# Kernel tuning notes

Hardware: AMD Instinct MI355X
Metric: run time of the kernel (lower is better)

The kernel has to match this reference:

```python
import jax, jax.numpy as jnp
import numpy as np

N, E, D, NHID, NOUT, G = 100000, 600000, 128, 512, 768, 2048
EPS = 1e-5

def _lin_init(k, fi, fo):
    s = 1.0 / np.sqrt(fi)
    kw, kb = jax.random.split(k)
    W = jax.random.uniform(kw, (fi, fo), jnp.float32, -s, s)
    b = jax.random.uniform(kb, (fo,), jnp.float32, -s, s)
    return W, b

def setup_inputs():
    key = jax.random.key(0)
    ks = jax.random.split(key, 16)
    inp = {}
    inp['x'] = jax.random.normal(ks[0], (N, D), jnp.float32)
    inp['edge_index'] = jax.random.randint(ks[1], (2, E), 0, N, jnp.int32)
    inp['batch'] = jnp.sort(jax.random.randint(ks[2], (N,), 0, G, jnp.int32))
    # 3 GCN layers + GAT attention layer + 4 MLP linears
    inp['W1'], inp['b1'] = _lin_init(ks[3], D, D)
    inp['W2'], inp['b2'] = _lin_init(ks[4], D, D)
    inp['W3'], inp['b3'] = _lin_init(ks[5], D, D)
    inp['Wa'], inp['ba'] = _lin_init(ks[6], D, D)
    ka1, ka2 = jax.random.split(ks[7])
    inp['a_src'] = jax.random.normal(ka1, (D,), jnp.float32) * 0.1
    inp['a_dst'] = jax.random.normal(ka2, (D,), jnp.float32) * 0.1
    # batchnorm affine params (4 BNs)
    for i, nm in enumerate(['g1', 'g2', 'g3', 'ga']):
        inp[nm] = jnp.ones((D,), jnp.float32)
        inp['be' + nm[1:]] = jnp.zeros((D,), jnp.float32)
    inp['Wl1'], inp['bl1'] = _lin_init(ks[8], D, NHID)
    inp['Wl2'], inp['bl2'] = _lin_init(ks[9], NHID, NHID)
    inp['Wl3'], inp['bl3'] = _lin_init(ks[10], NHID, NHID)
    inp['Wl4'], inp['bl4'] = _lin_init(ks[11], NHID, NOUT)
    inp['gln'] = jnp.ones((NOUT,), jnp.float32)
    inp['bln'] = jnp.zeros((NOUT,), jnp.float32)
    return inp

def _bn(x, g, b):
    # training-mode batchnorm over node dim (biased variance, like torch)
    mu = jnp.mean(x, axis=0)
    var = jnp.var(x, axis=0)
    return (x - mu) * jax.lax.rsqrt(var + EPS) * g + b

def _forward(x, edge_index, batch, W1, b1, g1, be1, W2, b2, g2, be2, W3, b3, g3, be3,
             Wa, ba, a_src, a_dst, ga, bea, Wl1, bl1, Wl2, bl2, Wl3, bl3, Wl4, bl4, gln, bln):
    loop = jnp.arange(N, dtype=edge_index.dtype)
    src = jnp.concatenate([edge_index[0], loop])  # [E+N] with self-loops
    dst = jnp.concatenate([edge_index[1], loop])
    deg = jax.ops.segment_sum(jnp.ones_like(dst, jnp.float32), dst, num_segments=N)
    dinv = jax.lax.rsqrt(deg)  # deg >= 1 thanks to self-loops
    norm = (dinv[src] * dinv[dst])[:, None]  # [E+N, 1]

    def gcn(h, W, b):
        h = h @ W
        return jax.ops.segment_sum(h[src] * norm, dst, num_segments=N) + b

    x = jax.nn.relu(_bn(gcn(x, W1, b1), g1, be1)) + x
    x = jax.nn.relu(_bn(gcn(x, W2, b2), g2, be2)) + x
    x = jax.nn.relu(_bn(gcn(x, W3, b3), g3, be3)) + x

    # GATConv, heads=1: edge logit = LeakyReLU(a_src.h_j + a_dst.h_i), softmax over dst
    h = x @ Wa
    al = h @ a_src  # [N]
    ar = h @ a_dst
    e = jax.nn.leaky_relu(al[src] + ar[dst], 0.2)  # [E+N]
    m = jax.ops.segment_max(e, dst, num_segments=N)
    ee = jnp.exp(e - m[dst])
    denom = jax.ops.segment_sum(ee, dst, num_segments=N)
    alpha = (ee / denom[dst])[:, None]
    x = jax.ops.segment_sum(alpha * h[src], dst, num_segments=N) + ba
    x = jax.nn.relu(_bn(x, ga, bea))

    # global_add_pool
    x = jax.ops.segment_sum(x, batch, num_segments=G)  # [G, D]

    x = jax.nn.relu(x @ Wl1 + bl1)
    x = jax.nn.relu(x @ Wl2 + bl2)
    x = jax.nn.relu(x @ Wl3 + bl3)
    x = x @ Wl4 + bl4
    mu = jnp.mean(x, axis=-1, keepdims=True)
    var = jnp.var(x, axis=-1, keepdims=True)
    return (x - mu) * jax.lax.rsqrt(var + EPS) * gln + bln

def reference(x, edge_index, batch, W1, b1, g1, be1, W2, b2, g2, be2, W3, b3, g3, be3,
              Wa, ba, a_src, a_dst, ga, bea, Wl1, bl1, Wl2, bl2, Wl3, bl3, Wl4, bl4, gln, bln):
    return _forward(x, edge_index, batch, W1, b1, g1, be1, W2, b2, g2, be2, W3, b3, g3, be3,
                    Wa, ba, a_src, a_dst, ga, bea, Wl1, bl1, Wl2, bl2, Wl3, bl3, Wl4, bl4, gln, bln)
```

## Files before the change

kernel.cpp:

```cpp
#include <hip/hip_runtime.h>
#include <cstdint>
#include <cstddef>

#define CDIV(a,b) (((a)+(b)-1)/(b))

constexpr int N_ = 100000;
constexpr int E_ = 600000;
constexpr int D_ = 128;
constexpr int G_ = 2048;
constexpr int NHID_ = 512;
constexpr int NOUT_ = 768;
constexpr float EPS_ = 1e-5f;
constexpr int AGG_BLOCKS = 2048;

typedef short bf16x8 __attribute__((ext_vector_type(8)));
typedef float f32x4 __attribute__((ext_vector_type(4)));

__device__ __forceinline__ float wave_sum(float v){
#pragma unroll
  for (int m = 32; m; m >>= 1) v += __shfl_xor(v, m, 64);
  return v;
}
__device__ __forceinline__ float lrelu02(float v){ return v > 0.f ? v : 0.2f * v; }
__device__ __forceinline__ unsigned short f2bf(float f){
  unsigned u = __float_as_uint(f);
  u += 0x7FFF + ((u >> 16) & 1);
  return (unsigned short)(u >> 16);
}
__device__ __forceinline__ float bflo(unsigned u){ return __uint_as_float(u << 16); }
__device__ __forceinline__ float bfhi(unsigned u){ return __uint_as_float(u & 0xFFFF0000u); }

__device__ __forceinline__ float4 unplo(uint4 u){ return make_float4(bflo(u.x), bflo(u.y), bflo(u.z), bflo(u.w)); }
__device__ __forceinline__ float4 unphi(uint4 u){ return make_float4(bfhi(u.x), bfhi(u.y), bfhi(u.z), bfhi(u.w)); }
__device__ __forceinline__ float4 bnrelu4(float4 v, float4 sc, float4 sh){
  return make_float4(fmaxf(v.x*sc.x+sh.x, 0.f), fmaxf(v.y*sc.y+sh.y, 0.f),
                     fmaxf(v.z*sc.z+sh.z, 0.f), fmaxf(v.w*sc.w+sh.w, 0.f));
}
__device__ __forceinline__ float4 add4(float4 a, float4 b){
  return make_float4(a.x+b.x, a.y+b.y, a.z+b.z, a.w+b.w);
}
__device__ __forceinline__ uint4 pk4(float4 lo, float4 hi){
  uint4 u;
  u.x = (unsigned)f2bf(lo.x) | ((unsigned)f2bf(hi.x) << 16);
  u.y = (unsigned)f2bf(lo.y) | ((unsigned)f2bf(hi.y) << 16);
  u.z = (unsigned)f2bf(lo.z) | ((unsigned)f2bf(hi.z) << 16);
  u.w = (unsigned)f2bf(lo.w) | ((unsigned)f2bf(hi.w) << 16);
  return u;
}
__device__ __forceinline__ bf16x8 mkaf(float4 lo, float4 hi){
  bf16x8 a;
  a[0]=(short)f2bf(lo.x); a[1]=(short)f2bf(lo.y); a[2]=(short)f2bf(lo.z); a[3]=(short)f2bf(lo.w);
  a[4]=(short)f2bf(hi.x); a[5]=(short)f2bf(hi.y); a[6]=(short)f2bf(hi.z); a[7]=(short)f2bf(hi.w);
  return a;
}
__device__ __forceinline__ bf16x8 mkaf_u(uint4 u){
  bf16x8 a;
  a[0]=(short)(u.x & 0xFFFF); a[4]=(short)(u.x >> 16);
  a[1]=(short)(u.y & 0xFFFF); a[5]=(short)(u.y >> 16);
  a[2]=(short)(u.z & 0xFFFF); a[6]=(short)(u.z >> 16);
  a[3]=(short)(u.w & 0xFFFF); a[7]=(short)(u.w >> 16);
  return a;
}

__global__ void k_count(const int* __restrict__ dst, int* __restrict__ cnt){
  int e = blockIdx.x * 256 + threadIdx.x;
  if (e < E_) atomicAdd(&cnt[dst[e]], 1);
}

__global__ void k_scan1(const int* __restrict__ cnt, int* __restrict__ ro, int* __restrict__ bs,
                        float* __restrict__ dinv){
  __shared__ int s[256];
  int tid = threadIdx.x;
  int i = blockIdx.x * 256 + tid;
  int v = (i < N_) ? cnt[i] : 0;
  s[tid] = v; __syncthreads();
  for (int off = 1; off < 256; off <<= 1){
    int add = (tid >= off) ? s[tid - off] : 0;
    __syncthreads();
    s[tid] += add;
    __syncthreads();
  }
  if (i < N_){
    ro[i] = s[tid] - v;
    dinv[i] = rsqrtf((float)(v + 1));
  }
  if (tid == 255) bs[blockIdx.x] = s[255];
}

__global__ void k_scan2(int* __restrict__ bs, int nb){
  __shared__ int s[512];
  int t = threadIdx.x;
  int v = (t < nb) ? bs[t] : 0;
  s[t] = v; __syncthreads();
  for (int off = 1; off < 512; off <<= 1){
    int a = (t >= off) ? s[t - off] : 0;
    __syncthreads();
    s[t] += a;
    __syncthreads();
  }
  if (t < nb) bs[t] = s[t] - v;
}

__global__ void k_scan3(int* __restrict__ ro, const int* __restrict__ bs){
  int i = blockIdx.x * 256 + threadIdx.x;
  if (i < N_) ro[i] += bs[i >> 8];
  if (i == N_) ro[N_] = E_;
}

__global__ void k_fill(const int* __restrict__ src, const int* __restrict__ dst,
                       const int* __restrict__ ro, int* __restrict__ cur, int* __restrict__ csr){
  int e = blockIdx.x * 256 + threadIdx.x;
  if (e < E_){
    int d = dst[e];
    int p = atomicAdd(&cur[d], 1);
    csr[ro[d] + p] = src[e];
  }
}

__global__ void k_bounds(const int* __restrict__ batch, int* __restrict__ gs){
  int g = blockIdx.x * 256 + threadIdx.x;
  if (g > G_) return;
  int lo = 0, hi = N_;
  while (lo < hi){ int mid = (lo + hi) >> 1; if (batch[mid] < g) lo = mid + 1; else hi = mid; }
  gs[g] = lo;
}

struct WprepArgs {
  const float* W[8];
  short* Wt[8];
  int K[8];
  int N[8];
  int ofs[9];
};

__global__ void k_wprep_all(WprepArgs a){
  int i = blockIdx.x * 256 + threadIdx.x;
  if (i >= a.ofs[8]) return;
  int m = 0;
  while (i >= a.ofs[m + 1]) ++m;
  int li = i - a.ofs[m];
  int K = a.K[m], Nn = a.N[m];
  int KT = K >> 5;
  int g = li & 3, t = (li >> 2) % KT, c = li / (KT * 4);
  short* o = a.Wt[m] + (size_t)li * 8;
  const float* W = a.W[m];
#pragma unroll
  for (int j = 0; j < 8; ++j){
    int k = t * 32 + (j >> 2) * 16 + g * 4 + (j & 3);
    o[j] = (short)f2bf(W[(size_t)k * Nn + c]);
  }
}

template<bool XB, bool RB>
__global__ __launch_bounds__(256) void k_mm_mfma(const void* __restrict__ Xin,
                                                 const short* __restrict__ Wt,
                                                 unsigned* __restrict__ hout,
                                                 const float* __restrict__ ss,
                                                 const void* __restrict__ resin,
                                                 unsigned* __restrict__ xnew,
                                                 const float* __restrict__ prescale,
                                                 const float* __restrict__ asrc,
                                                 const float* __restrict__ adst,
                                                 float* __restrict__ al_out,
                                                 float* __restrict__ ar_out){
  int lane = threadIdx.x & 63, wid = threadIdx.x >> 6;
  int cl = lane & 15, g = lane >> 4;
  int rw0 = blockIdx.x * 64 + wid * 16;
  int arow = rw0 + cl;
  bool rv = arow < N_;
  int rm = rv ? arow : 0;
  bool has_res = resin != nullptr;

  uint4 xu[4]; float4 xf[8];
  uint4 ru[4]; float4 rf[8];
  if (XB){
    const uint4* Xr = (const uint4*)((const unsigned*)Xin + (size_t)rm * 64);
#pragma unroll
    for (int t = 0; t < 4; ++t) xu[t] = Xr[t*4 + g];
  } else {
    const float4* Xr = (const float4*)((const float*)Xin + (size_t)rm * 128);
#pragma unroll
    for (int t = 0; t < 4; ++t){ xf[2*t] = Xr[t*8 + g]; xf[2*t+1] = Xr[t*8 + g + 4]; }
  }
  if (has_res){
    if (RB){
      const uint4* Rr = (const uint4*)((const unsigned*)resin + (size_t)rm * 64);
#pragma unroll
      for (int t = 0; t < 4; ++t) ru[t] = Rr[t*4 + g];
    } else {
      const float4* Rr = (const float4*)((const float*)resin + (size_t)rm * 128);
#pragma unroll
      for (int t = 0; t < 4; ++t){ rf[2*t] = Rr[t*8 + g]; rf[2*t+1] = Rr[t*8 + g + 4]; }
    }
  }
  __builtin_amdgcn_sched_barrier(0);

  bf16x8 af[4];
#pragma unroll
  for (int t = 0; t < 4; ++t){
    float4 lo, hi;
    if (XB){ lo = unplo(xu[t]); hi = unphi(xu[t]); }
    else    { lo = xf[2*t];     hi = xf[2*t+1];    }
    if (ss){
      int f0 = t * 32 + g * 4;
      float4 sc0 = *(const float4*)&ss[f0],      sh0 = *(const float4*)&ss[128 + f0];
      float4 sc1 = *(const float4*)&ss[f0 + 16], sh1 = *(const float4*)&ss[128 + f0 + 16];
      lo = bnrelu4(lo, sc0, sh0); hi = bnrelu4(hi, sc1, sh1);
      if (has_res){
        if (RB){ lo = add4(lo, unplo(ru[t])); hi = add4(hi, unphi(ru[t])); }
        else    { lo = add4(lo, rf[2*t]);     hi = add4(hi, rf[2*t+1]);    }
      }
      if (xnew && rv) *(uint4*)(xnew + (size_t)arow * 64 + t*16 + g*4) = pk4(lo, hi);
    }
    af[t] = mkaf(lo, hi);
  }

  f32x4 acc[8];
#pragma unroll
  for (int j = 0; j < 8; ++j) acc[j] = (f32x4){0,0,0,0};
#pragma unroll
  for (int t = 0; t < 4; ++t){
#pragma unroll
    for (int j = 0; j < 8; ++j){
      int c = j * 16 + cl;
      bf16x8 bf = *(const bf16x8*)(Wt + ((size_t)c * 16 + t * 4 + g) * 8);
      acc[j] = __builtin_amdgcn_mfma_f32_16x16x32_bf16(af[t], bf, acc[j], 0, 0, 0);
    }
  }

#pragma unroll
  for (int r = 0; r < 4; ++r){
    int row = rw0 + g * 4 + r;
    if (row < N_){
      float psc = prescale ? prescale[row] : 1.f;
#pragma unroll
      for (int jp = 0; jp < 4; ++jp){
        unsigned lo = f2bf(acc[2*jp][r] * psc);
        unsigned hi = f2bf(acc[2*jp+1][r] * psc);
        hout[(size_t)row * 64 + jp * 16 + cl] = (hi << 16) | lo;
      }
    }
  }

  if (al_out){
    float pal[4] = {0,0,0,0}, par[4] = {0,0,0,0};
#pragma unroll
    for (int j = 0; j < 8; ++j){
      float as_ = asrc[j * 16 + cl], ad_ = adst[j * 16 + cl];
#pragma unroll
      for (int r = 0; r < 4; ++r){ pal[r] += acc[j][r] * as_; par[r] += acc[j][r] * ad_; }
    }
#pragma unroll
    for (int m = 1; m < 16; m <<= 1)
#pragma unroll
      for (int r = 0; r < 4; ++r){
        pal[r] += __shfl_xor(pal[r], m, 64);
        par[r] += __shfl_xor(par[r], m, 64);
      }
    if (cl == 0){
#pragma unroll
      for (int r = 0; r < 4; ++r){
        int row = rw0 + g * 4 + r;
        if (row < N_){ al_out[row] = pal[r]; ar_out[row] = par[r]; }
      }
    }
  }
}

__global__ __launch_bounds__(256) void k_gcn_agg2(const unsigned* __restrict__ hbf, const int* __restrict__ ro,
                          const int* __restrict__ csr, const float* __restrict__ dinv,
                          const float* __restrict__ bias, unsigned* __restrict__ outb,
                          float4* __restrict__ pbuf){
  int wid = threadIdx.x >> 6, lane = threadIdx.x & 63;
  int f0 = 32 * (lane >> 4) + (lane & 15), f1 = f0 + 16;
  float bb0 = bias[f0], bb1 = bias[f1];
  float S0 = 0.f, S1 = 0.f, Q0 = 0.f, Q1 = 0.f;
  for (int node = blockIdx.x * 4 + wid; node < N_; node += AGG_BLOCKS * 4){
    int s0 = ro[node], s1 = ro[node + 1];
    int deg = s1 - s0;
    float di = dinv[node];
    unsigned us = hbf[(size_t)node * 64 + lane];
    float a0 = bflo(us), a1 = bfhi(us);
    if (deg <= 64){
      int sidx = (lane < deg) ? csr[s0 + lane] : 0;
      int j = 0;
      for (; j + 4 <= deg; j += 4){
        int sa = __shfl(sidx, j, 64),   sb = __shfl(sidx, j+1, 64);
        int sc = __shfl(sidx, j+2, 64), sd = __shfl(sidx, j+3, 64);
        unsigned ua = hbf[(size_t)sa*64+lane], ub = hbf[(size_t)sb*64+lane];
        unsigned uc = hbf[(size_t)sc*64+lane], ud = hbf[(size_t)sd*64+lane];
        a0 += bflo(ua) + bflo(ub) + bflo(uc) + bflo(ud);
        a1 += bfhi(ua) + bfhi(ub) + bfhi(uc) + bfhi(ud);
      }
      for (; j < deg; ++j){
        int s = __shfl(sidx, j, 64);
        unsigned u = hbf[(size_t)s*64+lane];
        a0 += bflo(u); a1 += bfhi(u);
      }
    } else {
      for (int base = s0; base < s1; base += 64){
        int c = min(64, s1 - base);
        int sidx = (lane < c) ? csr[base + lane] : 0;
        for (int j = 0; j < c; ++j){
          int s = __shfl(sidx, j, 64);
          unsigned u = hbf[(size_t)s*64+lane];
          a0 += bflo(u); a1 += bfhi(u);
        }
      }
    }
    float o0 = di * a0 + bb0;
    float o1 = di * a1 + bb1;
    outb[(size_t)node * 64 + lane] = (unsigned)f2bf(o0) | ((unsigned)f2bf(o1) << 16);
    S0 += o0; S1 += o1; Q0 += o0*o0; Q1 += o1*o1;
  }
  __shared__ float4 sred[4][64];
  sred[wid][lane] = make_float4(S0, S1, Q0, Q1);
  __syncthreads();
  if (wid == 0){
    float4 t = sred[0][lane];
    float4 u1 = sred[1][lane], u2 = sred[2][lane], u3 = sred[3][lane];
    t.x += u1.x + u2.x + u3.x;
    t.y += u1.y + u2.y + u3.y;
    t.z += u1.z + u2.z + u3.z;
    t.w += u1.w + u2.w + u3.w;
    pbuf[(size_t)blockIdx.x * 64 + lane] = t;
  }
}

__global__ __launch_bounds__(256) void k_gat_agg2(const unsigned* __restrict__ hbf, const int* __restrict__ ro,
                          const int* __restrict__ csr, const float* __restrict__ al,
                          const float* __restrict__ ar, const float* __restrict__ bias,
                          unsigned* __restrict__ outb, float4* __restrict__ pbuf){
  int wid = threadIdx.x >> 6, lane = threadIdx.x & 63;
  int f0 = 32 * (lane >> 4) + (lane & 15), f1 = f0 + 16;
  float bb0 = bias[f0], bb1 = bias[f1];
  float S0 = 0.f, S1 = 0.f, Q0 = 0.f, Q1 = 0.f;
  for (int node = blockIdx.x * 4 + wid; node < N_; node += AGG_BLOCKS * 4){
    int s0 = ro[node], s1 = ro[node + 1];
    int deg = s1 - s0;
    float ari = ar[node], ali = al[node];
    float pself = __expf(lrelu02(ali + ari));
    unsigned uself = hbf[(size_t)node * 64 + lane];
    float h0 = bflo(uself), h1 = bfhi(uself);
    float a0, a1;
    if (deg <= 64){
      int sidx = 0; float p = 0.f;
      if (lane < deg){ sidx = csr[s0 + lane]; p = __expf(lrelu02(al[sidx] + ari)); }
      float invd = 1.f / (wave_sum(p) + pself);
      float wl = p * invd;
      float wsf = pself * invd;
      a0 = wsf * h0; a1 = wsf * h1;
      int j = 0;
      for (; j + 4 <= deg; j += 4){
        int sa = __shfl(sidx, j, 64),   sb = __shfl(sidx, j+1, 64);
        int sc = __shfl(sidx, j+2, 64), sd = __shfl(sidx, j+3, 64);
        float wa = __shfl(wl, j, 64),   wb = __shfl(wl, j+1, 64);
        float wc = __shfl(wl, j+2, 64), wd = __shfl(wl, j+3, 64);
        unsigned ua = hbf[(size_t)sa*64+lane], ub = hbf[(size_t)sb*64+lane];
        unsigned uc = hbf[(size_t)sc*64+lane], ud = hbf[(size_t)sd*64+lane];
        a0 += wa*bflo(ua) + wb*bflo(ub) + wc*bflo(uc) + wd*bflo(ud);
        a1 += wa*bfhi(ua) + wb*bfhi(ub) + wc*bfhi(uc) + wd*bfhi(ud);
      }
      for (; j < deg; ++j){
        int s = __shfl(sidx, j, 64); float w = __shfl(wl, j, 64);
        unsigned u = hbf[(size_t)s*64+lane];
        a0 += w*bflo(u); a1 += w*bfhi(u);
      }
    } else {
      float denom = pself;
      for (int base = s0; base < s1; base += 64){
        int c = min(64, s1 - base);
        float p = 0.f;
        if (lane < c) p = __expf(lrelu02(al[csr[base + lane]] + ari));
        denom += wave_sum(p);
      }
      float invd = 1.f / denom;
      float wsf = pself * invd;
      a0 = wsf * h0; a1 = wsf * h1;
      for (int base = s0; base < s1; base += 64){
        int c = min(64, s1 - base);
        int sidx = 0; float wl = 0.f;
        if (lane < c){ sidx = csr[base + lane]; wl = __expf(lrelu02(al[sidx] + ari)) * invd; }
        for (int j = 0; j < c; ++j){
          int s = __shfl(sidx, j, 64); float w = __shfl(wl, j, 64);
          unsigned u = hbf[(size_t)s*64+lane];
          a0 += w*bflo(u); a1 += w*bfhi(u);
        }
      }
    }
    float o0 = a0 + bb0, o1 = a1 + bb1;
    outb[(size_t)node * 64 + lane] = (unsigned)f2bf(o0) | ((unsigned)f2bf(o1) << 16);
    S0 += o0; S1 += o1; Q0 += o0*o0; Q1 += o1*o1;
  }
  __shared__ float4 sred[4][64];
  sred[wid][lane] = make_float4(S0, S1, Q0, Q1);
  __syncthreads();
  if (wid == 0){
    float4 t = sred[0][lane];
    float4 u1 = sred[1][lane], u2 = sred[2][lane], u3 = sred[3][lane];
    t.x += u1.x + u2.x + u3.x;
    t.y += u1.y + u2.y + u3.y;
    t.z += u1.z + u2.z + u3.z;
    t.w += u1.w + u2.w + u3.w;
    pbuf[(size_t)blockIdx.x * 64 + lane] = t;
  }
}

__global__ void k_bn_reduce(const float4* __restrict__ pbuf, const float* __restrict__ g,
                            const float* __restrict__ be, float* __restrict__ ss){
  int c = blockIdx.x;
  int f0 = 32 * (c >> 4) + (c & 15), f1 = f0 + 16;
  float4 a = make_float4(0.f, 0.f, 0.f, 0.f);
  for (int r = threadIdx.x; r < AGG_BLOCKS; r += 256){
    float4 v = pbuf[(size_t)r * 64 + c];
    a.x += v.x; a.y += v.y; a.z += v.z; a.w += v.w;
  }
  __shared__ float4 s[256];
  s[threadIdx.x] = a; __syncthreads();
  for (int off = 128; off; off >>= 1){
    if (threadIdx.x < off){
      float4 o = s[threadIdx.x + off];
      s[threadIdx.x].x += o.x; s[threadIdx.x].y += o.y;
      s[threadIdx.x].z += o.z; s[threadIdx.x].w += o.w;
    }
    __syncthreads();
  }
  if (threadIdx.x == 0){
    float4 t = s[0];
    float inv_n = 1.f / (float)N_;
    float mean0 = t.x * inv_n, mean1 = t.y * inv_n;
    float var0 = fmaxf(t.z * inv_n - mean0 * mean0, 0.f);
    float var1 = fmaxf(t.w * inv_n - mean1 * mean1, 0.f);
    float sc0 = g[f0] * rsqrtf(var0 + EPS_);
    float sc1 = g[f1] * rsqrtf(var1 + EPS_);
    ss[f0] = sc0; ss[f1] = sc1;
    ss[128 + f0] = be[f0] - mean0 * sc0;
    ss[128 + f1] = be[f1] - mean1 * sc1;
  }
}

__global__ void k_pool2(const unsigned* __restrict__ xn, const int* __restrict__ gs,
                        const float* __restrict__ ss, unsigned* __restrict__ pooled){
  int g = blockIdx.x, f = threadIdx.x & 127, half = threadIdx.x >> 7;
  int idx = ((f >> 5) << 4) | (f & 15);
  int hi = (f >> 4) & 1;
  int s = gs[g], e = gs[g + 1];
  float sc = ss[f], sh = ss[128 + f];
  float a = 0.f;
  for (int n = s + half; n < e; n += 2){
    unsigned u = xn[(size_t)n * 64 + idx];
    float v = hi ? bfhi(u) : bflo(u);
    a += fmaxf(v * sc + sh, 0.f);
  }
  __shared__ float red[256];
  red[threadIdx.x] = a; __syncthreads();
  if (half == 0 && hi == 0){
    float vlo = red[f] + red[f + 128];
    float vhi = red[f + 16] + red[f + 16 + 128];
    pooled[(size_t)g * 64 + idx] = (unsigned)f2bf(vlo) | ((unsigned)f2bf(vhi) << 16);
  }
}

template<int K, bool RELU, bool OUTF32>
__global__ __launch_bounds__(256) void k_gemm_mfma(const unsigned* __restrict__ A,
                                                   const short* __restrict__ Wt,
                                                   const float* __restrict__ bias,
                                                   void* __restrict__ Cout, int Ncols){
  constexpr int KT = K >> 5;
  int lane = threadIdx.x & 63, wid = threadIdx.x >> 6;
  int cl = lane & 15, g = lane >> 4;
  int row0 = blockIdx.y * 64 + wid * 16;
  int cb = blockIdx.x;
  int arow = row0 + cl;
  const uint4* Ar = (const uint4*)(A + (size_t)arow * (K / 2));

  f32x4 acc[8];
#pragma unroll
  for (int j = 0; j < 8; ++j) acc[j] = (f32x4){0,0,0,0};

  for (int t = 0; t < KT; ++t){
    bf16x8 af = mkaf_u(Ar[t*4 + g]);
#pragma unroll
    for (int j = 0; j < 8; ++j){
      int c = cb * 128 + j * 16 + cl;
      bf16x8 bf = *(const bf16x8*)(Wt + (((size_t)c * KT + t) * 4 + g) * 8);
      acc[j] = __builtin_amdgcn_mfma_f32_16x16x32_bf16(af, bf, acc[j], 0, 0, 0);
    }
  }

  if (OUTF32){
    float* C = (float*)Cout;
#pragma unroll
    for (int r = 0; r < 4; ++r){
      int row = row0 + g * 4 + r;
#pragma unroll
      for (int j = 0; j < 8; ++j){
        int c = cb * 128 + j * 16 + cl;
        float v = acc[j][r] + bias[c];
        if (RELU) v = fmaxf(v, 0.f);
        C[(size_t)row * Ncols + c] = v;
      }
    }
  } else {
    unsigned* C = (unsigned*)Cout;
#pragma unroll
    for (int r = 0; r < 4; ++r){
      int row = row0 + g * 4 + r;
#pragma unroll
      for (int jp = 0; jp < 4; ++jp){
        int clo = cb * 128 + jp * 32 + cl;
        float vlo = acc[2*jp][r] + bias[clo];
        float vhi = acc[2*jp+1][r] + bias[clo + 16];
        if (RELU){ vlo = fmaxf(vlo, 0.f); vhi = fmaxf(vhi, 0.f); }
        C[(size_t)row * (Ncols / 2) + (cb * 4 + jp) * 16 + cl] =
            (unsigned)f2bf(vlo) | ((unsigned)f2bf(vhi) << 16);
      }
    }
  }
}

__global__ void k_layernorm(const float* __restrict__ xin, const float* __restrict__ g,
                            const float* __restrict__ b, float* __restrict__ out){
  __shared__ float red[8];
  int row = blockIdx.x, tid = threadIdx.x;
  float v0 = xin[(size_t)row*768 + tid];
  float v1 = xin[(size_t)row*768 + tid + 256];
  float v2 = xin[(size_t)row*768 + tid + 512];
  float s = v0 + v1 + v2;
  float q = v0*v0 + v1*v1 + v2*v2;
  s = wave_sum(s); q = wave_sum(q);
  int wid = tid >> 6;
  if ((tid & 63) == 0){ red[wid] = s; red[4 + wid] = q; }
  __syncthreads();
  if (tid == 0){
    float ts = red[0] + red[1] + red[2] + red[3];
    float tq = red[4] + red[5] + red[6] + red[7];
    float mean = ts / 768.f;
    float var = tq / 768.f - mean * mean;
    red[0] = mean; red[1] = rsqrtf(fmaxf(var, 0.f) + EPS_);
  }
  __syncthreads();
  float mean = red[0], inv = red[1];
  out[(size_t)row*768 + tid]       = (v0 - mean) * inv * g[tid]       + b[tid];
  out[(size_t)row*768 + tid + 256] = (v1 - mean) * inv * g[tid + 256] + b[tid + 256];
  out[(size_t)row*768 + tid + 512] = (v2 - mean) * inv * g[tid + 512] + b[tid + 512];
}

extern "C" void kernel_launch(void* const* d_in, const int* in_sizes, int n_in,
                              void* d_out, int out_size, void* d_ws, size_t ws_size,
                              hipStream_t stream){
  const float* x     = (const float*)d_in[0];
  const int*   ei    = (const int*)d_in[1];
  const int*   src   = ei;
  const int*   dst   = ei + E_;
  const int*   batch = (const int*)d_in[2];
  const float* W1 = (const float*)d_in[3];  const float* b1 = (const float*)d_in[4];
  const float* W2 = (const float*)d_in[5];  const float* b2 = (const float*)d_in[6];
  const float* W3 = (const float*)d_in[7];  const float* b3 = (const float*)d_in[8];
  const float* Wa = (const float*)d_in[9];  const float* ba = (const float*)d_in[10];
  const float* a_src = (const float*)d_in[11]; const float* a_dst = (const float*)d_in[12];
  const float* g1 = (const float*)d_in[13]; const float* be1 = (const float*)d_in[14];
  const float* g2 = (const float*)d_in[15]; const float* be2 = (const float*)d_in[16];
  const float* g3 = (const float*)d_in[17]; const float* be3 = (const float*)d_in[18];
  const float* ga = (const float*)d_in[19]; const float* bea = (const float*)d_in[20];
  const float* Wl1 = (const float*)d_in[21]; const float* bl1 = (const float*)d_in[22];
  const float* Wl2 = (const float*)d_in[23]; const float* bl2 = (const float*)d_in[24];
  const float* Wl3 = (const float*)d_in[25]; const float* bl3 = (const float*)d_in[26];
  const float* Wl4 = (const float*)d_in[27]; const float* bl4 = (const float*)d_in[28];
  const float* gln = (const float*)d_in[29]; const float* bln = (const float*)d_in[30];
  float* out = (float*)d_out;

  char* base = (char*)d_ws;
  size_t off = 0;
  auto alloc = [&](size_t bytes)->char*{
    char* p = base + off;
    off += (bytes + 255) & ~(size_t)255;
    return p;
  };
  int*   cnt    = (int*)  alloc((size_t)N_ * 4);
  float* dinv   = (float*)alloc((size_t)N_ * 4);
  int*   ro     = (int*)  alloc((size_t)(N_ + 1) * 4);
  int*   bs     = (int*)  alloc(512 * 4);
  int*   cur    = (int*)  alloc((size_t)N_ * 4);
  int*   csr    = (int*)  alloc((size_t)E_ * 4);
  int*   gstart = (int*)  alloc((size_t)(G_ + 1) * 4);
  float* al     = (float*)alloc((size_t)N_ * 4);
  float* ar     = (float*)alloc((size_t)N_ * 4);
  float* ss     = (float*)alloc(256 * 4);
  float4* pbuf  = (float4*)alloc((size_t)AGG_BLOCKS * 64 * 16);
  short* wt1    = (short*)alloc((size_t)128 * 128 * 2);
  short* wt2    = (short*)alloc((size_t)128 * 128 * 2);
  short* wt3    = (short*)alloc((size_t)128 * 128 * 2);
  short* wta    = (short*)alloc((size_t)128 * 128 * 2);
  short* wtl1   = (short*)alloc((size_t)128 * NHID_ * 2);
  short* wtl2   = (short*)alloc((size_t)NHID_ * NHID_ * 2);
  short* wtl3   = (short*)alloc((size_t)NHID_ * NHID_ * 2);
  short* wtl4   = (short*)alloc((size_t)NHID_ * NOUT_ * 2);
  unsigned* bufH  = (unsigned*)alloc((size_t)N_ * 64 * 4);
  unsigned* bufYb = (unsigned*)alloc((size_t)N_ * 64 * 4);
  unsigned* xresb = (unsigned*)alloc((size_t)N_ * 64 * 4);
  unsigned* pooled= (unsigned*)alloc((size_t)G_ * 64 * 4);
  unsigned* m1b   = (unsigned*)alloc((size_t)G_ * (NHID_/2) * 4);
  unsigned* m2b   = (unsigned*)alloc((size_t)G_ * (NHID_/2) * 4);
  float* m4     = (float*)alloc((size_t)G_ * NOUT_ * 4);
  (void)ws_size; (void)in_sizes; (void)n_in; (void)out_size;

  const int nbE = CDIV(E_, 256), nbN = CDIV(N_, 256);
  const int MMB = CDIV(N_, 64);

  hipMemsetAsync(cnt, 0, (size_t)N_ * 4, stream);
  k_count<<<nbE, 256, 0, stream>>>(dst, cnt);
  k_scan1<<<nbN, 256, 0, stream>>>(cnt, ro, bs, dinv);
  k_scan2<<<1, 512, 0, stream>>>(bs, nbN);
  k_scan3<<<CDIV(N_ + 1, 256), 256, 0, stream>>>(ro, bs);
  hipMemsetAsync(cur, 0, (size_t)N_ * 4, stream);
  k_fill<<<nbE, 256, 0, stream>>>(src, dst, ro, cur, csr);
  k_bounds<<<CDIV(G_ + 1, 256), 256, 0, stream>>>(batch, gstart);

  {
    WprepArgs a;
    const float* Ws[8] = {W1, W2, W3, Wa, Wl1, Wl2, Wl3, Wl4};
    short* Wts[8] = {wt1, wt2, wt3, wta, wtl1, wtl2, wtl3, wtl4};
    int Ks[8] = {128,128,128,128, 128, NHID_, NHID_, NHID_};
    int Ns[8] = {128,128,128,128, NHID_, NHID_, NHID_, NOUT_};
    int run = 0;
    for (int m = 0; m < 8; ++m){
      a.W[m] = Ws[m]; a.Wt[m] = Wts[m]; a.K[m] = Ks[m]; a.N[m] = Ns[m];
      a.ofs[m] = run;
      run += Ns[m] * (Ks[m] >> 5) * 4;
    }
    a.ofs[8] = run;
    k_wprep_all<<<CDIV(run, 256), 256, 0, stream>>>(a);
  }

  k_mm_mfma<false,false><<<MMB, 256, 0, stream>>>(x, wt1, bufH, nullptr, nullptr, nullptr,
                                                  dinv, nullptr, nullptr, nullptr, nullptr);
  k_gcn_agg2<<<AGG_BLOCKS, 256, 0, stream>>>(bufH, ro, csr, dinv, b1, bufYb, pbuf);
  k_bn_reduce<<<64, 256, 0, stream>>>(pbuf, g1, be1, ss);
  k_mm_mfma<true,false><<<MMB, 256, 0, stream>>>(bufYb, wt2, bufH, ss, x, xresb,
                                                 dinv, nullptr, nullptr, nullptr, nullptr);
  k_gcn_agg2<<<AGG_BLOCKS, 256, 0, stream>>>(bufH, ro, csr, dinv, b2, bufYb, pbuf);
  k_bn_reduce<<<64, 256, 0, stream>>>(pbuf, g2, be2, ss);
  k_mm_mfma<true,true><<<MMB, 256, 0, stream>>>(bufYb, wt3, bufH, ss, xresb, xresb,
                                                dinv, nullptr, nullptr, nullptr, nullptr);
  k_gcn_agg2<<<AGG_BLOCKS, 256, 0, stream>>>(bufH, ro, csr, dinv, b3, bufYb, pbuf);
  k_bn_reduce<<<64, 256, 0, stream>>>(pbuf, g3, be3, ss);
  k_mm_mfma<true,true><<<MMB, 256, 0, stream>>>(bufYb, wta, bufH, ss, xresb, nullptr,
                                                nullptr, a_src, a_dst, al, ar);
  k_gat_agg2<<<AGG_BLOCKS, 256, 0, stream>>>(bufH, ro, csr, al, ar, ba, bufYb, pbuf);
  k_bn_reduce<<<64, 256, 0, stream>>>(pbuf, ga, bea, ss);
  k_pool2<<<G_, 256, 0, stream>>>(bufYb, gstart, ss, pooled);
  k_gemm_mfma<128, true, false><<<dim3(NHID_/128, G_/64), 256, 0, stream>>>(pooled, wtl1, bl1, m1b, NHID_);
  k_gemm_mfma<512, true, false><<<dim3(NHID_/128, G_/64), 256, 0, stream>>>(m1b, wtl2, bl2, m2b, NHID_);
  k_gemm_mfma<512, true, false><<<dim3(NHID_/128, G_/64), 256, 0, stream>>>(m2b, wtl3, bl3, m1b, NHID_);
  k_gemm_mfma<512, false, true><<<dim3(NOUT_/128, G_/64), 256, 0, stream>>>(m1b, wtl4, bl4, m4, NOUT_);
  k_layernorm<<<G_, 256, 0, stream>>>(m4, gln, bln, out);
}
```

Measured before the change: 547.6 us.

## Make node GEMM persistent with register double-buffered prefetch of next tile

The per-node 128x128 MFMA GEMM kernel now launches a fixed grid of 521 blocks. Each block loops over 64-row tiles and prefetches the next tile's input and residual rows into registers while it computes the current one. This is meant to hide global load latency behind MFMA and epilogue work, and to cut block launch overhead. In exchange it doubles the register footprint for input buffers, which may lower occupancy, and with 1563 tiles over 521 blocks each block does exactly three iterations.

New measurement: 557.2 us. Within noise of the previous version (+1.7%).

```diff
diff --git a/kernel.cpp b/kernel.cpp
--- a/kernel.cpp
+++ b/kernel.cpp
@@ -12,6 +12,8 @@
 constexpr int NOUT_ = 768;
 constexpr float EPS_ = 1e-5f;
 constexpr int AGG_BLOCKS = 2048;
+constexpr int MM_NT = CDIV(N_, 64);
+constexpr int MM_GRID = 521;
 
 typedef short bf16x8 __attribute__((ext_vector_type(8)));
 typedef float f32x4 __attribute__((ext_vector_type(4)));
@@ -150,6 +152,38 @@
     o[j] = (short)f2bf(W[(size_t)k * Nn + c]);
   }
 }
+
+#define MM_LOADX(bt, xu, xf)                                                        \
+  do {                                                                              \
+    int arow_ = (bt) * 64 + wid * 16 + cl;                                          \
+    int rm_ = arow_ < N_ ? arow_ : 0;                                               \
+    if (XB){                                                                        \
+      const uint4* Xr_ = (const uint4*)((const unsigned*)Xin + (size_t)rm_ * 64);   \
+      _Pragma("unroll")                                                             \
+      for (int t_ = 0; t_ < 4; ++t_) xu[t_] = Xr_[t_*4 + g];                        \
+    } else {                                                                        \
+      const float4* Xr_ = (const float4*)((const float*)Xin + (size_t)rm_ * 128);   \
+      _Pragma("unroll")                                                             \
+      for (int t_ = 0; t_ < 4; ++t_){ xf[2*t_] = Xr_[t_*8 + g]; xf[2*t_+1] = Xr_[t_*8 + g + 4]; } \
+    }                                                                               \
+  } while(0)
+
+#define MM_LOADR(bt, ru, rf)                                                        \
+  do {                                                                              \
+    if (has_res){                                                                   \
+      int arow_ = (bt) * 64 + wid * 16 + cl;                                        \
+      int rm_ = arow_ < N_ ? arow_ : 0;                                             \
+      if (RB){                                                                      \
+        const uint4* Rr_ = (const uint4*)((const unsigned*)resin + (size_t)rm_ * 64);\
+        _Pragma("unroll")                                                           \
+        for (int t_ = 0; t_ < 4; ++t_) ru[t_] = Rr_[t_*4 + g];                      \
+      } else {                                                                      \
+        const float4* Rr_ = (const float4*)((const float*)resin + (size_t)rm_ * 128);\
+        _Pragma("unroll")                                                           \
+        for (int t_ = 0; t_ < 4; ++t_){ rf[2*t_] = Rr_[t_*8 + g]; rf[2*t_+1] = Rr_[t_*8 + g + 4]; } \
+      }                                                                             \
+    }                                                                               \
+  } while(0)
 
 template<bool XB, bool RB>
 __global__ __launch_bounds__(256) void k_mm_mfma(const void* __restrict__ Xin,
@@ -165,105 +199,105 @@
                                                  float* __restrict__ ar_out){
   int lane = threadIdx.x & 63, wid = threadIdx.x >> 6;
   int cl = lane & 15, g = lane >> 4;
-  int rw0 = blockIdx.x * 64 + wid * 16;
-  int arow = rw0 + cl;
-  bool rv = arow < N_;
-  int rm = rv ? arow : 0;
   bool has_res = resin != nullptr;
 
-  uint4 xu[4]; float4 xf[8];
-  uint4 ru[4]; float4 rf[8];
-  if (XB){
-    const uint4* Xr = (const uint4*)((const unsigned*)Xin + (size_t)rm * 64);
-#pragma unroll
-    for (int t = 0; t < 4; ++t) xu[t] = Xr[t*4 + g];
-  } else {
-    const float4* Xr = (const float4*)((const float*)Xin + (size_t)rm * 128);
-#pragma unroll
-    for (int t = 0; t < 4; ++t){ xf[2*t] = Xr[t*8 + g]; xf[2*t+1] = Xr[t*8 + g + 4]; }
-  }
-  if (has_res){
-    if (RB){
-      const uint4* Rr = (const uint4*)((const unsigned*)resin + (size_t)rm * 64);
-#pragma unroll
-      for (int t = 0; t < 4; ++t) ru[t] = Rr[t*4 + g];
-    } else {
-      const float4* Rr = (const float4*)((const float*)resin + (size_t)rm * 128);
-#pragma unroll
-      for (int t = 0; t < 4; ++t){ rf[2*t] = Rr[t*8 + g]; rf[2*t+1] = Rr[t*8 + g + 4]; }
-    }
-  }
-  __builtin_amdgcn_sched_barrier(0);
-
-  bf16x8 af[4];
-#pragma unroll
-  for (int t = 0; t < 4; ++t){
-    float4 lo, hi;
-    if (XB){ lo = unplo(xu[t]); hi = unphi(xu[t]); }
-    else    { lo = xf[2*t];     hi = xf[2*t+1];    }
-    if (ss){
-      int f0 = t * 32 + g * 4;
-      float4 sc0 = *(const float4*)&ss[f0],      sh0 = *(const float4*)&ss[128 + f0];
-      float4 sc1 = *(const float4*)&ss[f0 + 16], sh1 = *(const float4*)&ss[128 + f0 + 16];
-      lo = bnrelu4(lo, sc0, sh0); hi = bnrelu4(hi, sc1, sh1);
-      if (has_res){
-        if (RB){ lo = add4(lo, unplo(ru[t])); hi = add4(hi, unphi(ru[t])); }
-        else    { lo = add4(lo, rf[2*t]);     hi = add4(hi, rf[2*t+1]);    }
-      }
-      if (xnew && rv) *(uint4*)(xnew + (size_t)arow * 64 + t*16 + g*4) = pk4(lo, hi);
-    }
-    af[t] = mkaf(lo, hi);
-  }
-
-  f32x4 acc[8];
-#pragma unroll
-  for (int j = 0; j < 8; ++j) acc[j] = (f32x4){0,0,0,0};
-#pragma unroll
-  for (int t = 0; t < 4; ++t){
-#pragma unroll
-    for (int j = 0; j < 8; ++j){
-      int c = j * 16 + cl;
-      bf16x8 bf = *(const bf16x8*)(Wt + ((size_t)c * 16 + t * 4 + g) * 8);
-      acc[j] = __builtin_amdgcn_mfma_f32_16x16x32_bf16(af[t], bf, acc[j], 0, 0, 0);
-    }
-  }
-
-#pragma unroll
-  for (int r = 0; r < 4; ++r){
-    int row = rw0 + g * 4 + r;
-    if (row < N_){
-      float psc = prescale ? prescale[row] : 1.f;
-#pragma unroll
-      for (int jp = 0; jp < 4; ++jp){
-        unsigned lo = f2bf(acc[2*jp][r] * psc);
-        unsigned hi = f2bf(acc[2*jp+1][r] * psc);
-        hout[(size_t)row * 64 + jp * 16 + cl] = (hi << 16) | lo;
-      }
-    }
-  }
-
-  if (al_out){
-    float pal[4] = {0,0,0,0}, par[4] = {0,0,0,0};
-#pragma unroll
-    for (int j = 0; j < 8; ++j){
-      float as_ = asrc[j * 16 + cl], ad_ = adst[j * 16 + cl];
-#pragma unroll
-      for (int r = 0; r < 4; ++r){ pal[r] += acc[j][r] * as_; par[r] += acc[j][r] * ad_; }
-    }
-#pragma unroll
-    for (int m = 1; m < 16; m <<= 1)
-#pragma unroll
-      for (int r = 0; r < 4; ++r){
-        pal[r] += __shfl_xor(pal[r], m, 64);
-        par[r] += __shfl_xor(par[r], m, 64);
-      }
-    if (cl == 0){
-#pragma unroll
-      for (int r = 0; r < 4; ++r){
-        int row = rw0 + g * 4 + r;
-        if (row < N_){ al_out[row] = pal[r]; ar_out[row] = par[r]; }
-      }
-    }
+  uint4 cxu[4]; float4 cxf[8]; uint4 cru[4]; float4 crf[8];
+  uint4 nxu[4]; float4 nxf[8]; uint4 nru[4]; float4 nrf[8];
+
+  int bt = blockIdx.x;
+  MM_LOADX(bt, cxu, cxf);
+  MM_LOADR(bt, cru, crf);
+
+  for (;;){
+    int btn = bt + MM_GRID;
+    bool more = btn < MM_NT;
+    if (more){
+      MM_LOADX(btn, nxu, nxf);
+      MM_LOADR(btn, nru, nrf);
+    }
+    __builtin_amdgcn_sched_barrier(0);
+
+    int rw0 = bt * 64 + wid * 16;
+    int arow = rw0 + cl;
+    bool rv = arow < N_;
+
+    bf16x8 af[4];
+#pragma unroll
+    for (int t = 0; t < 4; ++t){
+      float4 lo, hi;
+      if (XB){ lo = unplo(cxu[t]); hi = unphi(cxu[t]); }
+      else    { lo = cxf[2*t];     hi = cxf[2*t+1];    }
+      if (ss){
+        int f0 = t * 32 + g * 4;
+        float4 sc0 = *(const float4*)&ss[f0],      sh0 = *(const float4*)&ss[128 + f0];
+        float4 sc1 = *(const float4*)&ss[f0 + 16], sh1 = *(const float4*)&ss[128 + f0 + 16];
+        lo = bnrelu4(lo, sc0, sh0); hi = bnrelu4(hi, sc1, sh1);
+        if (has_res){
+          if (RB){ lo = add4(lo, unplo(cru[t])); hi = add4(hi, unphi(cru[t])); }
+          else    { lo = add4(lo, crf[2*t]);     hi = add4(hi, crf[2*t+1]);    }
+        }
+        if (xnew && rv) *(uint4*)(xnew + (size_t)arow * 64 + t*16 + g*4) = pk4(lo, hi);
+      }
+      af[t] = mkaf(lo, hi);
+    }
+
+    f32x4 acc[8];
+#pragma unroll
+    for (int j = 0; j < 8; ++j) acc[j] = (f32x4){0,0,0,0};
+#pragma unroll
+    for (int t = 0; t < 4; ++t){
+#pragma unroll
+      for (int j = 0; j < 8; ++j){
+        int c = j * 16 + cl;
+        bf16x8 bf = *(const bf16x8*)(Wt + ((size_t)c * 16 + t * 4 + g) * 8);
+        acc[j] = __builtin_amdgcn_mfma_f32_16x16x32_bf16(af[t], bf, acc[j], 0, 0, 0);
+      }
+    }
+
+#pragma unroll
+    for (int r = 0; r < 4; ++r){
+      int row = rw0 + g * 4 + r;
+      if (row < N_){
+        float psc = prescale ? prescale[row] : 1.f;
+#pragma unroll
+        for (int jp = 0; jp < 4; ++jp){
+          unsigned lo = f2bf(acc[2*jp][r] * psc);
+          unsigned hi = f2bf(acc[2*jp+1][r] * psc);
+          hout[(size_t)row * 64 + jp * 16 + cl] = (hi << 16) | lo;
+        }
+      }
+    }
+
+    if (al_out){
+      float pal[4] = {0,0,0,0}, par[4] = {0,0,0,0};
+#pragma unroll
+      for (int j = 0; j < 8; ++j){
+        float as_ = asrc[j * 16 + cl], ad_ = adst[j * 16 + cl];
+#pragma unroll
+        for (int r = 0; r < 4; ++r){ pal[r] += acc[j][r] * as_; par[r] += acc[j][r] * ad_; }
+      }
+#pragma unroll
+      for (int m = 1; m < 16; m <<= 1)
+#pragma unroll
+        for (int r = 0; r < 4; ++r){
+          pal[r] += __shfl_xor(pal[r], m, 64);
+          par[r] += __shfl_xor(par[r], m, 64);
+        }
+      if (cl == 0){
+#pragma unroll
+        for (int r = 0; r < 4; ++r){
+          int row = rw0 + g * 4 + r;
+          if (row < N_){ al_out[row] = pal[r]; ar_out[row] = par[r]; }
+        }
+      }
+    }
+
+    if (!more) break;
+    bt = btn;
+#pragma unroll
+    for (int t = 0; t < 4; ++t){ cxu[t] = nxu[t]; cru[t] = nru[t]; }
+#pragma unroll
+    for (int i = 0; i < 8; ++i){ cxf[i] = nxf[i]; crf[i] = nrf[i]; }
   }
 }
 
@@ -606,7 +640,6 @@
   (void)ws_size; (void)in_sizes; (void)n_in; (void)out_size;
 
   const int nbE = CDIV(E_, 256), nbN = CDIV(N_, 256);
-  const int MMB = CDIV(N_, 64);
 
   hipMemsetAsync(cnt, 0, (size_t)N_ * 4, stream);
   k_count<<<nbE, 256, 0, stream>>>(dst, cnt);
@@ -633,20 +666,20 @@
     k_wprep_all<<<CDIV(run, 256), 256, 0, stream>>>(a);
   }
 
-  k_mm_mfma<false,false><<<MMB, 256, 0, stream>>>(x, wt1, bufH, nullptr, nullptr, nullptr,
-                                                  dinv, nullptr, nullptr, nullptr, nullptr);
+  k_mm_mfma<false,false><<<MM_GRID, 256, 0, stream>>>(x, wt1, bufH, nullptr, nullptr, nullptr,
+                                                      dinv, nullptr, nullptr, nullptr, nullptr);
   k_gcn_agg2<<<AGG_BLOCKS, 256, 0, stream>>>(bufH, ro, csr, dinv, b1, bufYb, pbuf);
   k_bn_reduce<<<64, 256, 0, stream>>>(pbuf, g1, be1, ss);
-  k_mm_mfma<true,false><<<MMB, 256, 0, stream>>>(bufYb, wt2, bufH, ss, x, xresb,
-                                                 dinv, nullptr, nullptr, nullptr, nullptr);
+  k_mm_mfma<true,false><<<MM_GRID, 256, 0, stream>>>(bufYb, wt2, bufH, ss, x, xresb,
+                                                     dinv, nullptr, nullptr, nullptr, nullptr);
   k_gcn_agg2<<<AGG_BLOCKS, 256, 0, stream>>>(bufH, ro, csr, dinv, b2, bufYb, pbuf);
   k_bn_reduce<<<64, 256, 0, stream>>>(pbuf, g2, be2, ss);
-  k_mm_mfma<true,true><<<MMB, 256, 0, stream>>>(bufYb, wt3, bufH, ss, xresb, xresb,
-                                                dinv, nullptr, nullptr, nullptr, nullptr);
+  k_mm_mfma<true,true><<<MM_GRID, 256, 0, stream>>>(bufYb, wt3, bufH, ss, xresb, xresb,
+                                                    dinv, nullptr, nullptr, nullptr, nullptr);
   k_gcn_agg2<<<AGG_BLOCKS, 256, 0, stream>>>(bufH, ro, csr, dinv, b3, bufYb, pbuf);
   k_bn_reduce<<<64, 256, 0, stream>>>(pbuf, g3, be3, ss);
-  k_mm_mfma<true,true><<<MMB, 256, 0, stream>>>(bufYb, wta, bufH, ss, xresb, nullptr,
-                                                nullptr, a_src, a_dst, al, ar);
+  k_mm_mfma<true,true><<<MM_GRID, 256, 0, stream>>>(bufYb, wta, bufH, ss, xresb, nullptr,
+                                                    nullptr, a_src, a_dst, al, ar);
   k_gat_agg2<<<AGG_BLOCKS, 256, 0, stream>>>(bufH, ro, csr, al, ar, ba, bufYb, pbuf);
   k_bn_reduce<<<64, 256, 0, stream>>>(pbuf, ga, bea, ss);
   k_pool2<<<G_, 256, 0, stream>>>(bufYb, gstart, ss, pooled);
```
